# Optimization experiments

Hardware: AMD Instinct MI355X
Metric: run time of the kernel (lower is better)

## Reference

```python
import jax, jax.numpy as jnp
import numpy as np

REACH = 2
BS = 32  # blocksize
NHID = 15  # nlayers - 1
CI = 12    # 2*(reach+1)*reach


def _offsets():
    # matches get_nb ordering: rows above (dy=-2,-1; dx=-2..2), then left (dy=0; dx=-2,-1)
    offs = [(dy, dx) for dy in range(-REACH, 0) for dx in range(-REACH, REACH + 1)]
    offs += [(0, dx) for dx in range(-REACH, 0)]
    return offs


def setup_inputs() -> dict:
    key = jax.random.key(0)
    k0, k1, k2, k3, k4 = jax.random.split(key, 5)
    x = jax.random.uniform(k0, (8, 3, 512, 512), jnp.float32, -1.0, 1.0)
    s = 1.0 / np.sqrt(CI).astype(np.float32)
    Wh = jax.random.uniform(k1, (NHID, CI, CI), jnp.float32, -s, s)
    bh = jax.random.uniform(k2, (NHID, CI), jnp.float32, -s, s)
    Wo = jax.random.uniform(k3, (1, CI), jnp.float32, -s, s)
    bo = jax.random.uniform(k4, (1,), jnp.float32, -s, s)
    return {"x": x, "Wh": Wh, "bh": bh, "Wo": Wo, "bo": bo}


def reference(x, Wh, bh, Wo, bo):
    b, c, h, w = x.shape
    h = h // BS * BS
    w = w // BS * BS
    x = x[:, :, :h, :w]
    nbh, nbw = h // BS, w // BS
    # unfold into (nbc, BS, BS) blocks, matching torch unfold/unfold/reshape
    blocks = x.reshape(b, c, nbh, BS, nbw, BS).transpose(0, 1, 2, 4, 3, 5).reshape(-1, BS, BS)
    xp = jnp.pad(blocks, ((0, 0), (REACH, REACH), (REACH, REACH)))
    # batched causal-neighbor gather: (nbc, BS, BS, 12)
    feats = jnp.stack(
        [xp[:, REACH + dy:REACH + dy + BS, REACH + dx:REACH + dx + BS] for dy, dx in _offsets()],
        axis=-1,
    )
    hdn = feats
    for l in range(NHID):
        hdn = jax.nn.leaky_relu(jnp.einsum('nhwi,oi->nhwo', hdn, Wh[l]) + bh[l])
    pred = jnp.clip(jnp.einsum('nhwi,oi->nhwo', hdn, Wo)[..., 0] + bo[0], -1.0, 1.0)
    deltas = jnp.fmod(blocks - pred + 1.0, 2.0) - 1.0
    deltas = deltas.reshape(b * c, h * w)
    loss1 = 255.0 * jnp.sqrt(jnp.mean(jnp.square(deltas)))
    return (loss1, deltas)
```

## Files before the change

### kernel.cpp

```cpp
#include <hip/hip_runtime.h>
#include <math.h>

#define CI 12
#define NHID 15
#define NBLK 6144
#define NPIX (NBLK * 1024)

typedef int i32x4 __attribute__((ext_vector_type(4)));

static __device__ __forceinline__ int bfpack(float lo, float hi) {
    return (int)__builtin_amdgcn_perm(__float_as_uint(hi), __float_as_uint(lo),
                                      0x07060302u);
}
static __device__ __forceinline__ unsigned bfrne(float x) {
    unsigned u = __float_as_uint(x);
    u += 0x7FFFu + ((u >> 16) & 1u);
    return u >> 16;
}
static __device__ __forceinline__ int bfpack_rne(float lo, float hi) {
    return (int)((bfrne(hi) << 16) | bfrne(lo));
}

#define LKA \
  "v_mul_f32 v68, 0x3c23d70a, v52\n" \
  "v_mul_f32 v69, 0x3c23d70a, v53\n" \
  "v_max_f32 v52, v52, v68\n" \
  "v_max_f32 v53, v53, v69\n" \
  "v_perm_b32 v36, v53, v52, s20\n" \
  "v_mul_f32 v68, 0x3c23d70a, v54\n" \
  "v_mul_f32 v69, 0x3c23d70a, v55\n" \
  "v_max_f32 v54, v54, v68\n" \
  "v_max_f32 v55, v55, v69\n" \
  "v_perm_b32 v37, v55, v54, s20\n"
#define LKB \
  "v_mul_f32 v68, 0x3c23d70a, v56\n" \
  "v_mul_f32 v69, 0x3c23d70a, v57\n" \
  "v_max_f32 v56, v56, v68\n" \
  "v_max_f32 v57, v57, v69\n" \
  "v_perm_b32 v40, v57, v56, s20\n" \
  "v_mul_f32 v68, 0x3c23d70a, v58\n" \
  "v_mul_f32 v69, 0x3c23d70a, v59\n" \
  "v_max_f32 v58, v58, v68\n" \
  "v_max_f32 v59, v59, v69\n" \
  "v_perm_b32 v41, v59, v58, s20\n"
#define LKC \
  "v_mul_f32 v68, 0x3c23d70a, v60\n" \
  "v_mul_f32 v69, 0x3c23d70a, v61\n" \
  "v_max_f32 v60, v60, v68\n" \
  "v_max_f32 v61, v61, v69\n" \
  "v_perm_b32 v44, v61, v60, s20\n" \
  "v_mul_f32 v68, 0x3c23d70a, v62\n" \
  "v_mul_f32 v69, 0x3c23d70a, v63\n" \
  "v_max_f32 v62, v62, v68\n" \
  "v_max_f32 v63, v63, v69\n" \
  "v_perm_b32 v45, v63, v62, s20\n"
#define LKD \
  "v_mul_f32 v68, 0x3c23d70a, v64\n" \
  "v_mul_f32 v69, 0x3c23d70a, v65\n" \
  "v_max_f32 v64, v64, v68\n" \
  "v_max_f32 v65, v65, v69\n" \
  "v_perm_b32 v48, v65, v64, s20\n" \
  "v_mul_f32 v68, 0x3c23d70a, v66\n" \
  "v_mul_f32 v69, 0x3c23d70a, v67\n" \
  "v_max_f32 v66, v66, v68\n" \
  "v_max_f32 v67, v67, v69\n" \
  "v_perm_b32 v49, v67, v66, s20\n"

#define MFA(w) "v_mfma_f32_16x16x32_bf16 v[52:55], %[" w "], v[36:39], v[32:35]\n"
#define MFB(w) "v_mfma_f32_16x16x32_bf16 v[56:59], %[" w "], v[40:43], v[32:35]\n"
#define MFC(w) "v_mfma_f32_16x16x32_bf16 v[60:63], %[" w "], v[44:47], v[32:35]\n"
#define MFD(w) "v_mfma_f32_16x16x32_bf16 v[64:67], %[" w "], v[48:51], v[32:35]\n"

#define LAYER(w) LKA LKB MFA(w) LKC MFB(w) LKD MFC(w) "s_nop 1\n" MFD(w)

__global__ __launch_bounds__(256, 3) void codec_main(
    const float* __restrict__ x,
    const float* __restrict__ Wh,
    const float* __restrict__ bh,
    const float* __restrict__ Wo,
    const float* __restrict__ bo,
    float* __restrict__ out,
    float* __restrict__ loss_acc)
{
    __shared__ float tile[36 * 37];
    __shared__ float stage[4][256];
    __shared__ float wsum[4];

    const int n    = blockIdx.x;
    const int tid  = threadIdx.x;
    const int lane = tid & 63;
    const int wv   = tid >> 6;
    const int t    = lane & 15;
    const int q    = lane >> 4;

    {
        const int col = tid & 31;
        const int r0  = tid >> 5;
        #pragma unroll
        for (int i = 0; i < 6; ++i) {
            int idx = tid + i * 256;
            if (idx < 36 * 37) tile[idx] = 0.0f;
        }
        __syncthreads();
        const int bc  = n >> 8;
        const int blk = n & 255;
        const int by  = blk >> 4;
        const int bx  = blk & 15;
        #pragma unroll
        for (int p = 0; p < 4; ++p) {
            const int row = r0 + 8 * p;
            tile[(row + 2) * 37 + col + 2] =
                x[((size_t)bc * 512 + (size_t)(by * 32 + row)) * 512
                  + (size_t)(bx * 32 + col)];
        }
        __syncthreads();
    }

    i32x4 wq[16];
    const bool wok = (t < CI) && (q < 3);
    #pragma unroll
    for (int l = 0; l < NHID; ++l) {
        float4 w = {0.f, 0.f, 0.f, 0.f};
        float  b = 0.f;
        if (wok) w = *(const float4*)(Wh + l * (CI * CI) + t * CI + 4 * q);
        if (wok && q == 0) b = bh[l * CI + t];
        wq[l] = (i32x4){ bfpack_rne(w.x, w.y), bfpack_rne(w.z, w.w),
                         bfpack_rne(b, 0.f), 0 };
    }
    {
        float4 w = {0.f, 0.f, 0.f, 0.f};
        float  b = 0.f;
        if (t == 0 && q < 3) w = *(const float4*)(Wo + 4 * q);
        if (t == 0 && q == 0) b = bo[0];
        wq[15] = (i32x4){ bfpack_rne(w.x, w.y), bfpack_rne(w.z, w.w),
                          bfpack_rne(b, 0.f), 0 };
    }

    const int sh8  = q * 8;
    const int off0 = (int)(signed char)((0x00DCB8B4u >> sh8) & 0xFFu);
    const int off1 = (int)(signed char)((0x00DDD9B5u >> sh8) & 0xFFu);
    const int off2 = (int)(signed char)((0x00FEDAB6u >> sh8) & 0xFFu);
    const int off3 = (int)(signed char)((0x00FFDBB7u >> sh8) & 0xFFu);

    const int biasreg = (q == 0) ? 0x00003F80 : 0;
    int e = (wv * 8 + 2) * 37 + (t + 2);

    float d2 = 0.0f;
    #pragma unroll 1
    for (int yi = 0; yi < 4; ++yi) {
        const int faA0 = bfpack(tile[e + off0],      tile[e + off1]);
        const int faA1 = bfpack(tile[e + off2],      tile[e + off3]);
        const int fbA0 = bfpack(tile[e + off0 + 16], tile[e + off1 + 16]);
        const int fbA1 = bfpack(tile[e + off2 + 16], tile[e + off3 + 16]);
        const int fcA0 = bfpack(tile[e + off0 + 37], tile[e + off1 + 37]);
        const int fcA1 = bfpack(tile[e + off2 + 37], tile[e + off3 + 37]);
        const int fdA0 = bfpack(tile[e + off0 + 53], tile[e + off1 + 53]);
        const int fdA1 = bfpack(tile[e + off2 + 53], tile[e + off3 + 53]);
        const float vA = tile[e], vB = tile[e + 16];
        const float vC = tile[e + 37], vD = tile[e + 53];

        float pA, pB, pC, pD;
        asm volatile(
            "s_mov_b32 s20, 0x07060302\n"
            "v_mov_b32 v32, 0\n" "v_mov_b32 v33, 0\n"
            "v_mov_b32 v34, 0\n" "v_mov_b32 v35, 0\n"
            "v_mov_b32 v36, %[fa0]\n" "v_mov_b32 v37, %[fa1]\n"
            "v_mov_b32 v38, %[bias]\n" "v_mov_b32 v39, 0\n"
            "v_mov_b32 v40, %[fb0]\n" "v_mov_b32 v41, %[fb1]\n"
            "v_mov_b32 v42, %[bias]\n" "v_mov_b32 v43, 0\n"
            "v_mov_b32 v44, %[fc0]\n" "v_mov_b32 v45, %[fc1]\n"
            "v_mov_b32 v46, %[bias]\n" "v_mov_b32 v47, 0\n"
            "v_mov_b32 v48, %[fd0]\n" "v_mov_b32 v49, %[fd1]\n"
            "v_mov_b32 v50, %[bias]\n" "v_mov_b32 v51, 0\n"
            MFA("w0") MFB("w0") MFC("w0") MFD("w0")
            "s_nop 7\n" "s_nop 7\n" "s_nop 7\n"
            LAYER("w1")  LAYER("w2")  LAYER("w3")  LAYER("w4")
            LAYER("w5")  LAYER("w6")  LAYER("w7")  LAYER("w8")
            LAYER("w9")  LAYER("w10") LAYER("w11") LAYER("w12")
            LAYER("w13") LAYER("w14") LAYER("w15")
            "v_mov_b32 %[pA], v52\n"
            "v_mov_b32 %[pB], v56\n"
            "s_nop 7\n" "s_nop 7\n"
            "v_mov_b32 %[pC], v60\n"
            "s_nop 3\n"
            "v_mov_b32 %[pD], v64\n"
            : [pA] "=v"(pA), [pB] "=v"(pB), [pC] "=v"(pC), [pD] "=v"(pD)
            : [w0] "a"(wq[0]),  [w1] "a"(wq[1]),  [w2] "a"(wq[2]),
              [w3] "a"(wq[3]),  [w4] "a"(wq[4]),  [w5] "a"(wq[5]),
              [w6] "a"(wq[6]),  [w7] "a"(wq[7]),  [w8] "a"(wq[8]),
              [w9] "a"(wq[9]),  [w10] "a"(wq[10]), [w11] "a"(wq[11]),
              [w12] "a"(wq[12]), [w13] "a"(wq[13]), [w14] "a"(wq[14]),
              [w15] "a"(wq[15]),
              [fa0] "v"(faA0), [fa1] "v"(faA1), [fb0] "v"(fbA0), [fb1] "v"(fbA1),
              [fc0] "v"(fcA0), [fc1] "v"(fcA1), [fd0] "v"(fdA0), [fd1] "v"(fdA1),
              [bias] "v"(biasreg)
            : "s20",
              "v32","v33","v34","v35","v36","v37","v38","v39",
              "v40","v41","v42","v43","v44","v45","v46","v47",
              "v48","v49","v50","v51","v52","v53","v54","v55",
              "v56","v57","v58","v59","v60","v61","v62","v63",
              "v64","v65","v66","v67","v68","v69");

        if (lane < 16) {
            const float qA = fminf(fmaxf(pA, -1.0f), 1.0f);
            const float uA = vA - qA + 1.0f;
            const float dA = uA - ((uA < 2.0f) ? 1.0f : 3.0f);
            const float qB = fminf(fmaxf(pB, -1.0f), 1.0f);
            const float uB = vB - qB + 1.0f;
            const float dB = uB - ((uB < 2.0f) ? 1.0f : 3.0f);
            const float qC = fminf(fmaxf(pC, -1.0f), 1.0f);
            const float uC = vC - qC + 1.0f;
            const float dC = uC - ((uC < 2.0f) ? 1.0f : 3.0f);
            const float qD = fminf(fmaxf(pD, -1.0f), 1.0f);
            const float uD = vD - qD + 1.0f;
            const float dD = uD - ((uD < 2.0f) ? 1.0f : 3.0f);
            const int r = 2 * yi;
            stage[wv][r * 32 + t]            = dA;
            stage[wv][r * 32 + 16 + t]       = dB;
            stage[wv][(r + 1) * 32 + t]      = dC;
            stage[wv][(r + 1) * 32 + 16 + t] = dD;
            d2 = fmaf(dA, dA, fmaf(dB, dB, fmaf(dC, dC, fmaf(dD, dD, d2))));
        }
        e += 74;
    }

    float* outp = out + 1 + (size_t)n * 1024 + wv * 256;
    #pragma unroll
    for (int j = 0; j < 4; ++j)
        outp[j * 64 + lane] = stage[wv][j * 64 + lane];

    #pragma unroll
    for (int off = 8; off > 0; off >>= 1) d2 += __shfl_down(d2, off, 64);
    if (lane == 0) wsum[wv] = d2;
    __syncthreads();
    if (tid == 0) atomicAdd(loss_acc, wsum[0] + wsum[1] + wsum[2] + wsum[3]);
}

__global__ void codec_loss(const float* __restrict__ acc, float* __restrict__ out)
{
    out[0] = 255.0f * sqrtf(acc[0] / (float)NPIX);
}

extern "C" void kernel_launch(void* const* d_in, const int* in_sizes, int n_in,
                              void* d_out, int out_size, void* d_ws, size_t ws_size,
                              hipStream_t stream)
{
    const float* x  = (const float*)d_in[0];
    const float* Wh = (const float*)d_in[1];
    const float* bh = (const float*)d_in[2];
    const float* Wo = (const float*)d_in[3];
    const float* bo = (const float*)d_in[4];
    float* out = (float*)d_out;
    float* acc = (float*)d_ws;

    hipMemsetAsync(acc, 0, sizeof(float), stream);
    codec_main<<<NBLK, 256, 0, stream>>>(x, Wh, bh, Wo, bo, out, acc);
    codec_loss<<<1, 1, 0, stream>>>(acc, out);
}
```

Before: 219.6 us.

## Switch MLP MFMAs to fp16 with packed activations and fuse loss finalization

Result: slower. 378.7 us (+72.4%).

```diff
diff --git a/kernel.cpp b/kernel.cpp
--- a/kernel.cpp
+++ b/kernel.cpp
@@ -7,71 +7,32 @@
 #define NPIX (NBLK * 1024)
 
 typedef int i32x4 __attribute__((ext_vector_type(4)));
-
-static __device__ __forceinline__ int bfpack(float lo, float hi) {
-    return (int)__builtin_amdgcn_perm(__float_as_uint(hi), __float_as_uint(lo),
-                                      0x07060302u);
+typedef _Float16 h2 __attribute__((ext_vector_type(2)));
+
+static __device__ __forceinline__ int pkrtz(float lo, float hi) {
+    return __builtin_bit_cast(int, __builtin_amdgcn_cvt_pkrtz(lo, hi));
 }
-static __device__ __forceinline__ unsigned bfrne(float x) {
-    unsigned u = __float_as_uint(x);
-    u += 0x7FFFu + ((u >> 16) & 1u);
-    return u >> 16;
-}
-static __device__ __forceinline__ int bfpack_rne(float lo, float hi) {
-    return (int)((bfrne(hi) << 16) | bfrne(lo));
-}
-
-#define LKA \
-  "v_mul_f32 v68, 0x3c23d70a, v52\n" \
-  "v_mul_f32 v69, 0x3c23d70a, v53\n" \
-  "v_max_f32 v52, v52, v68\n" \
-  "v_max_f32 v53, v53, v69\n" \
-  "v_perm_b32 v36, v53, v52, s20\n" \
-  "v_mul_f32 v68, 0x3c23d70a, v54\n" \
-  "v_mul_f32 v69, 0x3c23d70a, v55\n" \
-  "v_max_f32 v54, v54, v68\n" \
-  "v_max_f32 v55, v55, v69\n" \
-  "v_perm_b32 v37, v55, v54, s20\n"
-#define LKB \
-  "v_mul_f32 v68, 0x3c23d70a, v56\n" \
-  "v_mul_f32 v69, 0x3c23d70a, v57\n" \
-  "v_max_f32 v56, v56, v68\n" \
-  "v_max_f32 v57, v57, v69\n" \
-  "v_perm_b32 v40, v57, v56, s20\n" \
-  "v_mul_f32 v68, 0x3c23d70a, v58\n" \
-  "v_mul_f32 v69, 0x3c23d70a, v59\n" \
-  "v_max_f32 v58, v58, v68\n" \
-  "v_max_f32 v59, v59, v69\n" \
-  "v_perm_b32 v41, v59, v58, s20\n"
-#define LKC \
-  "v_mul_f32 v68, 0x3c23d70a, v60\n" \
-  "v_mul_f32 v69, 0x3c23d70a, v61\n" \
-  "v_max_f32 v60, v60, v68\n" \
-  "v_max_f32 v61, v61, v69\n" \
-  "v_perm_b32 v44, v61, v60, s20\n" \
-  "v_mul_f32 v68, 0x3c23d70a, v62\n" \
-  "v_mul_f32 v69, 0x3c23d70a, v63\n" \
-  "v_max_f32 v62, v62, v68\n" \
-  "v_max_f32 v63, v63, v69\n" \
-  "v_perm_b32 v45, v63, v62, s20\n"
-#define LKD \
-  "v_mul_f32 v68, 0x3c23d70a, v64\n" \
-  "v_mul_f32 v69, 0x3c23d70a, v65\n" \
-  "v_max_f32 v64, v64, v68\n" \
-  "v_max_f32 v65, v65, v69\n" \
-  "v_perm_b32 v48, v65, v64, s20\n" \
-  "v_mul_f32 v68, 0x3c23d70a, v66\n" \
-  "v_mul_f32 v69, 0x3c23d70a, v67\n" \
-  "v_max_f32 v66, v66, v68\n" \
-  "v_max_f32 v67, v67, v69\n" \
-  "v_perm_b32 v49, v67, v66, s20\n"
-
-#define MFA(w) "v_mfma_f32_16x16x32_bf16 v[52:55], %[" w "], v[36:39], v[32:35]\n"
-#define MFB(w) "v_mfma_f32_16x16x32_bf16 v[56:59], %[" w "], v[40:43], v[32:35]\n"
-#define MFC(w) "v_mfma_f32_16x16x32_bf16 v[60:63], %[" w "], v[44:47], v[32:35]\n"
-#define MFD(w) "v_mfma_f32_16x16x32_bf16 v[64:67], %[" w "], v[48:51], v[32:35]\n"
-
-#define LAYER(w) LKA LKB MFA(w) LKC MFB(w) LKD MFC(w) "s_nop 1\n" MFD(w)
+
+#define ACT(d0, d1, b) \
+  "v_cvt_pkrtz_f16_f32 v68, " d0 ", " d1 "\n" \
+  "v_pk_mul_f16 v69, v70, v68\n" \
+  "v_pk_max_f16 " b ", v68, v69\n"
+
+#define MFA(w) "v_mfma_f32_16x16x32_f16 v[52:55], %[" w "], v[36:39], v[32:35]\n"
+#define MFB(w) "v_mfma_f32_16x16x32_f16 v[56:59], %[" w "], v[40:43], v[32:35]\n"
+#define MFC(w) "v_mfma_f32_16x16x32_f16 v[60:63], %[" w "], v[44:47], v[32:35]\n"
+#define MFD(w) "v_mfma_f32_16x16x32_f16 v[64:67], %[" w "], v[48:51], v[32:35]\n"
+
+#define LAYER(w) \
+  ACT("v52","v53","v36") ACT("v54","v55","v37") \
+  ACT("v56","v57","v40") ACT("v58","v59","v41") \
+  MFA(w) \
+  ACT("v60","v61","v44") ACT("v62","v63","v45") \
+  MFB(w) \
+  ACT("v64","v65","v48") ACT("v66","v67","v49") \
+  MFC(w) \
+  "s_nop 1\n" \
+  MFD(w)
 
 __global__ __launch_bounds__(256, 3) void codec_main(
     const float* __restrict__ x,
@@ -80,7 +41,8 @@
     const float* __restrict__ Wo,
     const float* __restrict__ bo,
     float* __restrict__ out,
-    float* __restrict__ loss_acc)
+    float* __restrict__ loss_acc,
+    unsigned* __restrict__ done_cnt)
 {
     __shared__ float tile[36 * 37];
     __shared__ float stage[4][256];
@@ -124,16 +86,14 @@
         float  b = 0.f;
         if (wok) w = *(const float4*)(Wh + l * (CI * CI) + t * CI + 4 * q);
         if (wok && q == 0) b = bh[l * CI + t];
-        wq[l] = (i32x4){ bfpack_rne(w.x, w.y), bfpack_rne(w.z, w.w),
-                         bfpack_rne(b, 0.f), 0 };
+        wq[l] = (i32x4){ pkrtz(w.x, w.y), pkrtz(w.z, w.w), pkrtz(b, 0.f), 0 };
     }
     {
         float4 w = {0.f, 0.f, 0.f, 0.f};
         float  b = 0.f;
         if (t == 0 && q < 3) w = *(const float4*)(Wo + 4 * q);
         if (t == 0 && q == 0) b = bo[0];
-        wq[15] = (i32x4){ bfpack_rne(w.x, w.y), bfpack_rne(w.z, w.w),
-                          bfpack_rne(b, 0.f), 0 };
+        wq[15] = (i32x4){ pkrtz(w.x, w.y), pkrtz(w.z, w.w), pkrtz(b, 0.f), 0 };
     }
 
     const int sh8  = q * 8;
@@ -142,47 +102,45 @@
     const int off2 = (int)(signed char)((0x00FEDAB6u >> sh8) & 0xFFu);
     const int off3 = (int)(signed char)((0x00FFDBB7u >> sh8) & 0xFFu);
 
-    const int biasreg = (q == 0) ? 0x00003F80 : 0;
+    const int biasreg = (q == 0) ? 0x00003C00 : 0;
     int e = (wv * 8 + 2) * 37 + (t + 2);
 
     float d2 = 0.0f;
     #pragma unroll 1
     for (int yi = 0; yi < 4; ++yi) {
-        const int faA0 = bfpack(tile[e + off0],      tile[e + off1]);
-        const int faA1 = bfpack(tile[e + off2],      tile[e + off3]);
-        const int fbA0 = bfpack(tile[e + off0 + 16], tile[e + off1 + 16]);
-        const int fbA1 = bfpack(tile[e + off2 + 16], tile[e + off3 + 16]);
-        const int fcA0 = bfpack(tile[e + off0 + 37], tile[e + off1 + 37]);
-        const int fcA1 = bfpack(tile[e + off2 + 37], tile[e + off3 + 37]);
-        const int fdA0 = bfpack(tile[e + off0 + 53], tile[e + off1 + 53]);
-        const int fdA1 = bfpack(tile[e + off2 + 53], tile[e + off3 + 53]);
+        const int fa0 = pkrtz(tile[e + off0],      tile[e + off1]);
+        const int fa1 = pkrtz(tile[e + off2],      tile[e + off3]);
+        const int fb0 = pkrtz(tile[e + off0 + 16], tile[e + off1 + 16]);
+        const int fb1 = pkrtz(tile[e + off2 + 16], tile[e + off3 + 16]);
+        const int fc0 = pkrtz(tile[e + off0 + 37], tile[e + off1 + 37]);
+        const int fc1 = pkrtz(tile[e + off2 + 37], tile[e + off3 + 37]);
+        const int fd0 = pkrtz(tile[e + off0 + 53], tile[e + off1 + 53]);
+        const int fd1 = pkrtz(tile[e + off2 + 53], tile[e + off3 + 53]);
         const float vA = tile[e], vB = tile[e + 16];
         const float vC = tile[e + 37], vD = tile[e + 53];
 
         float pA, pB, pC, pD;
         asm volatile(
-            "s_mov_b32 s20, 0x07060302\n"
+            "v_mov_b32 v70, 0x211f211f\n"
             "v_mov_b32 v32, 0\n" "v_mov_b32 v33, 0\n"
             "v_mov_b32 v34, 0\n" "v_mov_b32 v35, 0\n"
+            "v_mov_b32 v38, %[bias]\n" "v_mov_b32 v39, 0\n"
+            "v_mov_b32 v42, %[bias]\n" "v_mov_b32 v43, 0\n"
+            "v_mov_b32 v46, %[bias]\n" "v_mov_b32 v47, 0\n"
+            "v_mov_b32 v50, %[bias]\n" "v_mov_b32 v51, 0\n"
             "v_mov_b32 v36, %[fa0]\n" "v_mov_b32 v37, %[fa1]\n"
-            "v_mov_b32 v38, %[bias]\n" "v_mov_b32 v39, 0\n"
             "v_mov_b32 v40, %[fb0]\n" "v_mov_b32 v41, %[fb1]\n"
-            "v_mov_b32 v42, %[bias]\n" "v_mov_b32 v43, 0\n"
             "v_mov_b32 v44, %[fc0]\n" "v_mov_b32 v45, %[fc1]\n"
-            "v_mov_b32 v46, %[bias]\n" "v_mov_b32 v47, 0\n"
             "v_mov_b32 v48, %[fd0]\n" "v_mov_b32 v49, %[fd1]\n"
-            "v_mov_b32 v50, %[bias]\n" "v_mov_b32 v51, 0\n"
             MFA("w0") MFB("w0") MFC("w0") MFD("w0")
-            "s_nop 7\n" "s_nop 7\n" "s_nop 7\n"
             LAYER("w1")  LAYER("w2")  LAYER("w3")  LAYER("w4")
             LAYER("w5")  LAYER("w6")  LAYER("w7")  LAYER("w8")
             LAYER("w9")  LAYER("w10") LAYER("w11") LAYER("w12")
             LAYER("w13") LAYER("w14") LAYER("w15")
+            "s_nop 7\n" "s_nop 7\n" "s_nop 7\n"
             "v_mov_b32 %[pA], v52\n"
             "v_mov_b32 %[pB], v56\n"
-            "s_nop 7\n" "s_nop 7\n"
             "v_mov_b32 %[pC], v60\n"
-            "s_nop 3\n"
             "v_mov_b32 %[pD], v64\n"
             : [pA] "=v"(pA), [pB] "=v"(pB), [pC] "=v"(pC), [pD] "=v"(pD)
             : [w0] "a"(wq[0]),  [w1] "a"(wq[1]),  [w2] "a"(wq[2]),
@@ -191,15 +149,14 @@
               [w9] "a"(wq[9]),  [w10] "a"(wq[10]), [w11] "a"(wq[11]),
               [w12] "a"(wq[12]), [w13] "a"(wq[13]), [w14] "a"(wq[14]),
               [w15] "a"(wq[15]),
-              [fa0] "v"(faA0), [fa1] "v"(faA1), [fb0] "v"(fbA0), [fb1] "v"(fbA1),
-              [fc0] "v"(fcA0), [fc1] "v"(fcA1), [fd0] "v"(fdA0), [fd1] "v"(fdA1),
+              [fa0] "v"(fa0), [fa1] "v"(fa1), [fb0] "v"(fb0), [fb1] "v"(fb1),
+              [fc0] "v"(fc0), [fc1] "v"(fc1), [fd0] "v"(fd0), [fd1] "v"(fd1),
               [bias] "v"(biasreg)
-            : "s20",
-              "v32","v33","v34","v35","v36","v37","v38","v39",
+            : "v32","v33","v34","v35","v36","v37","v38","v39",
               "v40","v41","v42","v43","v44","v45","v46","v47",
               "v48","v49","v50","v51","v52","v53","v54","v55",
               "v56","v57","v58","v59","v60","v61","v62","v63",
-              "v64","v65","v66","v67","v68","v69");
+              "v64","v65","v66","v67","v68","v69","v70");
 
         if (lane < 16) {
             const float qA = fminf(fmaxf(pA, -1.0f), 1.0f);
@@ -233,12 +190,18 @@
     for (int off = 8; off > 0; off >>= 1) d2 += __shfl_down(d2, off, 64);
     if (lane == 0) wsum[wv] = d2;
     __syncthreads();
-    if (tid == 0) atomicAdd(loss_acc, wsum[0] + wsum[1] + wsum[2] + wsum[3]);
-}
-
-__global__ void codec_loss(const float* __restrict__ acc, float* __restrict__ out)
-{
-    out[0] = 255.0f * sqrtf(acc[0] / (float)NPIX);
+    if (tid == 0) {
+        const float s = wsum[0] + wsum[1] + wsum[2] + wsum[3];
+        __hip_atomic_fetch_add(loss_acc, s, __ATOMIC_RELEASE,
+                               __HIP_MEMORY_SCOPE_AGENT);
+        const unsigned old = __hip_atomic_fetch_add(done_cnt, 1u,
+                               __ATOMIC_ACQ_REL, __HIP_MEMORY_SCOPE_AGENT);
+        if (old == NBLK - 1) {
+            const float tot = __hip_atomic_load(loss_acc, __ATOMIC_ACQUIRE,
+                                                __HIP_MEMORY_SCOPE_AGENT);
+            out[0] = 255.0f * sqrtf(tot / (float)NPIX);
+        }
+    }
 }
 
 extern "C" void kernel_launch(void* const* d_in, const int* in_sizes, int n_in,
@@ -251,9 +214,9 @@
     const float* Wo = (const float*)d_in[3];
     const float* bo = (const float*)d_in[4];
     float* out = (float*)d_out;
-    float* acc = (float*)d_ws;
-
-    hipMemsetAsync(acc, 0, sizeof(float), stream);
-    codec_main<<<NBLK, 256, 0, stream>>>(x, Wh, bh, Wo, bo, out, acc);
-    codec_loss<<<1, 1, 0, stream>>>(acc, out);
+    float*    acc = (float*)d_ws;
+    unsigned* cnt = (unsigned*)d_ws + 1;
+
+    hipMemsetAsync(d_ws, 0, 8, stream);
+    codec_main<<<NBLK, 256, 0, stream>>>(x, Wh, bh, Wo, bo, out, acc, cnt);
 }
```
